# Kernel optimization log

Hardware: AMD Instinct MI355X
Metric: run time of the kernel (lower is better)

Reference implementation:

```python
import jax, jax.numpy as jnp
import numpy as np

B, O, GRID = 2048, 48, 112
SIGMA = 5.0


def setup_inputs() -> dict:
    key = jax.random.key(0)
    k1, k2, k3, k4, k5 = jax.random.split(key, 5)
    s = float(GRID - 1)
    xL = jax.random.uniform(k1, (B,), dtype=jnp.float32) * s
    yL = jax.random.uniform(k2, (B,), dtype=jnp.float32) * s
    obj_list = jax.random.uniform(k3, (B, O, 2), dtype=jnp.float32) * s
    obj_num = jax.random.randint(k4, (B,), 0, O + 1, dtype=jnp.int32)
    road_mask = jax.random.randint(k5, (B, GRID, GRID), 0, 2, dtype=jnp.int32)
    return {"xL": xL, "yL": yL, "obj_list": obj_list, "obj_num": obj_num,
            "road_mask": road_mask, "H": GRID, "W": GRID}


def reference(xL, yL, obj_list, obj_num, road_mask, H, W):
    # Faithful vectorization of batch_gaussian_tensor_obj.
    # exp(-(dx^2+dy^2)/(2s^2)) is separable: exp(-dx^2/..) * exp(-dy^2/..),
    # so per-object splats reduce to a batched matmul over the object axis.
    inv = 1.0 / (2.0 * SIGMA * SIGMA)
    x = jnp.arange(H, dtype=jnp.float32)  # row coordinate grid
    y = jnp.arange(W, dtype=jnp.float32)  # col coordinate grid

    # positive goal gaussian, rank-1 outer product per batch element
    gx = jnp.exp(-((x[None, :] - xL[:, None]) ** 2) * inv)  # [B,H]
    gy = jnp.exp(-((y[None, :] - yL[:, None]) ** 2) * inv)  # [B,W]
    goal = gx[:, :, None] * gy[:, None, :]                   # [B,H,W]

    # negative object gaussians; note original swaps xy: xo=xy[1], yo=xy[0]
    xo = obj_list[:, :, 1]  # [B,O] row coords
    yo = obj_list[:, :, 0]  # [B,O] col coords
    ex = jnp.exp(-((x[None, None, :] - xo[:, :, None]) ** 2) * inv)  # [B,O,H]
    ey = jnp.exp(-((y[None, None, :] - yo[:, :, None]) ** 2) * inv)  # [B,O,W]
    valid = (jnp.arange(O)[None, :] < obj_num[:, None]).astype(jnp.float32)  # [B,O]
    obj = jnp.einsum('boh,bow->bhw', ex * valid[:, :, None], ey)     # [B,H,W]

    channel = 0.5 + 0.5 * goal - 0.5 * obj
    channel = jnp.where(road_mask == 0, 0.0, channel)
    return channel
```

## Files before the change

### kernel.cpp

```cpp
#include <hip/hip_runtime.h>

#define GRID_N 112
#define O_MAX 48
#define HW_N (GRID_N * GRID_N)
#define NT 128
#define ROWS_MAX (O_MAX + 1)

typedef _Float16 half4_t __attribute__((ext_vector_type(4)));
typedef _Float16 half8_t __attribute__((ext_vector_type(8)));

__global__ __launch_bounds__(NT) void goalmap_kernel(
    const float* __restrict__ xL, const float* __restrict__ yL,
    const float* __restrict__ obj_list, const int* __restrict__ obj_num,
    const int* __restrict__ road_mask, float* __restrict__ out)
{
    constexpr float INV = 1.0f / (2.0f * 5.0f * 5.0f);

    __shared__ _Float16 sex[ROWS_MAX * GRID_N];
    __shared__ _Float16 sey[ROWS_MAX * GRID_N];

    const int b   = blockIdx.x;
    const int tid = threadIdx.x;
    const int n   = obj_num[b];
    const int rows = n + 1;
    const float xl = xL[b];
    const float yl = yL[b];

    for (int i = tid; i < rows * GRID_N; i += NT) {
        int o = i / GRID_N;
        int p = i - o * GRID_N;
        float cx, cy, sgn;
        if (o < n) {
            cx  = obj_list[(b * O_MAX + o) * 2 + 1];
            cy  = obj_list[(b * O_MAX + o) * 2 + 0];
            sgn = -0.5f;
        } else {
            cx  = xl;
            cy  = yl;
            sgn = 0.5f;
        }
        float dx = (float)p - cx;
        float dy = (float)p - cy;
        sex[i] = (_Float16)(sgn * __expf(-dx * dx * INV));
        sey[i] = (_Float16)(__expf(-dy * dy * INV));
    }
    __syncthreads();

    const int* rm = road_mask + (size_t)b * HW_N;
    float*     op = out       + (size_t)b * HW_N;

    const int NTILES = (GRID_N / 4) * (GRID_N / 8);
    for (int t = tid; t < NTILES; t += NT) {
        int hp = t / 14;
        int wq = t - hp * 14;
        int h = hp * 4;
        int w = wq * 8;

        float acc[4][8];
        #pragma unroll
        for (int r = 0; r < 4; ++r)
            #pragma unroll
            for (int c = 0; c < 8; ++c) acc[r][c] = 0.f;

        #pragma unroll 2
        for (int o = 0; o < rows; ++o) {
            half4_t ex4 = *(const half4_t*)&sex[o * GRID_N + h];
            half8_t ey8 = *(const half8_t*)&sey[o * GRID_N + w];
            float ef[4], gf[8];
            #pragma unroll
            for (int r = 0; r < 4; ++r) ef[r] = (float)ex4[r];
            #pragma unroll
            for (int c = 0; c < 8; ++c) gf[c] = (float)ey8[c];
            #pragma unroll
            for (int r = 0; r < 4; ++r)
                #pragma unroll
                for (int c = 0; c < 8; ++c)
                    acc[r][c] = fmaf(ef[r], gf[c], acc[r][c]);
        }

        #pragma unroll
        for (int r = 0; r < 4; ++r) {
            int base = (h + r) * GRID_N + w;
            int4 m0 = *(const int4*)&rm[base];
            int4 m1 = *(const int4*)&rm[base + 4];
            float4 v0, v1;
            v0.x = 0.5f + acc[r][0];
            v0.y = 0.5f + acc[r][1];
            v0.z = 0.5f + acc[r][2];
            v0.w = 0.5f + acc[r][3];
            v1.x = 0.5f + acc[r][4];
            v1.y = 0.5f + acc[r][5];
            v1.z = 0.5f + acc[r][6];
            v1.w = 0.5f + acc[r][7];
            v0.x = (m0.x == 0) ? 0.f : v0.x;
            v0.y = (m0.y == 0) ? 0.f : v0.y;
            v0.z = (m0.z == 0) ? 0.f : v0.z;
            v0.w = (m0.w == 0) ? 0.f : v0.w;
            v1.x = (m1.x == 0) ? 0.f : v1.x;
            v1.y = (m1.y == 0) ? 0.f : v1.y;
            v1.z = (m1.z == 0) ? 0.f : v1.z;
            v1.w = (m1.w == 0) ? 0.f : v1.w;
            *(float4*)&op[base]     = v0;
            *(float4*)&op[base + 4] = v1;
        }
    }
}

extern "C" void kernel_launch(void* const* d_in, const int* in_sizes, int n_in,
                              void* d_out, int out_size, void* d_ws, size_t ws_size,
                              hipStream_t stream) {
    const float* xL        = (const float*)d_in[0];
    const float* yL        = (const float*)d_in[1];
    const float* obj_list  = (const float*)d_in[2];
    const int*   obj_num   = (const int*)d_in[3];
    const int*   road_mask = (const int*)d_in[4];
    float*       out       = (float*)d_out;
    const int B = in_sizes[0];

    goalmap_kernel<<<B, NT, 0, stream>>>(xL, yL, obj_list, obj_num, road_mask, out);
}
```

Measured before the change: 222.0 us.

## Compute object splat sum with MFMA 16x16x32 f16 over transposed LDS tiles

Replaces the scalar FMA outer-product accumulation with MFMA matrix instructions. Exponential tables are stored transposed as [position][object] and zero-padded to 64 objects, so each 16x16 output tile takes two MFMA ops. The block size is doubled and work is assigned one tile per wavefront. Every batch element now pays for 64 object slots even when it has few objects, and the stores become scalar per lane, one row segment of 16 floats per quad, which may reduce store coalescing compared with the previous float4 writes.

```diff
diff --git a/kernel.cpp b/kernel.cpp
--- a/kernel.cpp
+++ b/kernel.cpp
@@ -3,11 +3,13 @@
 #define GRID_N 112
 #define O_MAX 48
 #define HW_N (GRID_N * GRID_N)
-#define NT 128
-#define ROWS_MAX (O_MAX + 1)
+#define NT 256
+#define KPAD 64
+#define LSTR 72
 
-typedef _Float16 half4_t __attribute__((ext_vector_type(4)));
-typedef _Float16 half8_t __attribute__((ext_vector_type(8)));
+typedef _Float16 half8  __attribute__((ext_vector_type(8)));
+typedef _Float16 half2v __attribute__((ext_vector_type(2)));
+typedef float    f32x4  __attribute__((ext_vector_type(4)));
 
 __global__ __launch_bounds__(NT) void goalmap_kernel(
     const float* __restrict__ xL, const float* __restrict__ yL,
@@ -16,92 +18,72 @@
 {
     constexpr float INV = 1.0f / (2.0f * 5.0f * 5.0f);
 
-    __shared__ _Float16 sex[ROWS_MAX * GRID_N];
-    __shared__ _Float16 sey[ROWS_MAX * GRID_N];
+    __shared__ _Float16 exT[GRID_N * LSTR];
+    __shared__ _Float16 eyT[GRID_N * LSTR];
 
     const int b   = blockIdx.x;
     const int tid = threadIdx.x;
     const int n   = obj_num[b];
-    const int rows = n + 1;
     const float xl = xL[b];
     const float yl = yL[b];
+    const float* ob = obj_list + (size_t)b * O_MAX * 2;
 
-    for (int i = tid; i < rows * GRID_N; i += NT) {
-        int o = i / GRID_N;
-        int p = i - o * GRID_N;
-        float cx, cy, sgn;
-        if (o < n) {
-            cx  = obj_list[(b * O_MAX + o) * 2 + 1];
-            cy  = obj_list[(b * O_MAX + o) * 2 + 0];
-            sgn = -0.5f;
-        } else {
-            cx  = xl;
-            cy  = yl;
-            sgn = 0.5f;
+    for (int i = tid; i < GRID_N * (KPAD / 2); i += NT) {
+        int pos = i >> 5;
+        int o0  = (i & 31) * 2;
+        half2v vx, vy;
+        #pragma unroll
+        for (int j = 0; j < 2; ++j) {
+            int o = o0 + j;
+            float valx = 0.f, valy = 0.f;
+            if (o <= n) {
+                float cx, cy, s;
+                if (o < n) { cx = ob[o * 2 + 1]; cy = ob[o * 2 + 0]; s = -0.5f; }
+                else       { cx = xl;            cy = yl;            s =  0.5f; }
+                float dx = (float)pos - cx;
+                float dy = (float)pos - cy;
+                valx = s * __expf(-dx * dx * INV);
+                valy =     __expf(-dy * dy * INV);
+            }
+            vx[j] = (_Float16)valx;
+            vy[j] = (_Float16)valy;
         }
-        float dx = (float)p - cx;
-        float dy = (float)p - cy;
-        sex[i] = (_Float16)(sgn * __expf(-dx * dx * INV));
-        sey[i] = (_Float16)(__expf(-dy * dy * INV));
+        *(half2v*)&exT[pos * LSTR + o0] = vx;
+        *(half2v*)&eyT[pos * LSTR + o0] = vy;
     }
     __syncthreads();
 
     const int* rm = road_mask + (size_t)b * HW_N;
     float*     op = out       + (size_t)b * HW_N;
 
-    const int NTILES = (GRID_N / 4) * (GRID_N / 8);
-    for (int t = tid; t < NTILES; t += NT) {
-        int hp = t / 14;
-        int wq = t - hp * 14;
-        int h = hp * 4;
-        int w = wq * 8;
+    const int lane = tid & 63;
+    const int wid  = tid >> 6;
+    const int m    = lane & 15;
+    const int quad = lane >> 4;
 
-        float acc[4][8];
-        #pragma unroll
-        for (int r = 0; r < 4; ++r)
-            #pragma unroll
-            for (int c = 0; c < 8; ++c) acc[r][c] = 0.f;
+    for (int t = wid; t < 49; t += 4) {
+        int th = t / 7;
+        int tw = t - th * 7;
 
-        #pragma unroll 2
-        for (int o = 0; o < rows; ++o) {
-            half4_t ex4 = *(const half4_t*)&sex[o * GRID_N + h];
-            half8_t ey8 = *(const half8_t*)&sey[o * GRID_N + w];
-            float ef[4], gf[8];
-            #pragma unroll
-            for (int r = 0; r < 4; ++r) ef[r] = (float)ex4[r];
-            #pragma unroll
-            for (int c = 0; c < 8; ++c) gf[c] = (float)ey8[c];
-            #pragma unroll
-            for (int r = 0; r < 4; ++r)
-                #pragma unroll
-                for (int c = 0; c < 8; ++c)
-                    acc[r][c] = fmaf(ef[r], gf[c], acc[r][c]);
-        }
+        const _Float16* arow = &exT[(th * 16 + m) * LSTR + quad * 8];
+        const _Float16* brow = &eyT[(tw * 16 + m) * LSTR + quad * 8];
+        half8 a0 = *(const half8*)arow;
+        half8 b0 = *(const half8*)brow;
+        half8 a1 = *(const half8*)(arow + 32);
+        half8 b1 = *(const half8*)(brow + 32);
 
+        f32x4 acc = {0.f, 0.f, 0.f, 0.f};
+        acc = __builtin_amdgcn_mfma_f32_16x16x32_f16(a0, b0, acc, 0, 0, 0);
+        acc = __builtin_amdgcn_mfma_f32_16x16x32_f16(a1, b1, acc, 0, 0, 0);
+
+        int h0 = th * 16 + quad * 4;
+        int w0 = tw * 16 + m;
         #pragma unroll
         for (int r = 0; r < 4; ++r) {
-            int base = (h + r) * GRID_N + w;
-            int4 m0 = *(const int4*)&rm[base];
-            int4 m1 = *(const int4*)&rm[base + 4];
-            float4 v0, v1;
-            v0.x = 0.5f + acc[r][0];
-            v0.y = 0.5f + acc[r][1];
-            v0.z = 0.5f + acc[r][2];
-            v0.w = 0.5f + acc[r][3];
-            v1.x = 0.5f + acc[r][4];
-            v1.y = 0.5f + acc[r][5];
-            v1.z = 0.5f + acc[r][6];
-            v1.w = 0.5f + acc[r][7];
-            v0.x = (m0.x == 0) ? 0.f : v0.x;
-            v0.y = (m0.y == 0) ? 0.f : v0.y;
-            v0.z = (m0.z == 0) ? 0.f : v0.z;
-            v0.w = (m0.w == 0) ? 0.f : v0.w;
-            v1.x = (m1.x == 0) ? 0.f : v1.x;
-            v1.y = (m1.y == 0) ? 0.f : v1.y;
-            v1.z = (m1.z == 0) ? 0.f : v1.z;
-            v1.w = (m1.w == 0) ? 0.f : v1.w;
-            *(float4*)&op[base]     = v0;
-            *(float4*)&op[base + 4] = v1;
+            int idx = (h0 + r) * GRID_N + w0;
+            int mv = rm[idx];
+            float v = 0.5f + acc[r];
+            op[idx] = (mv == 0) ? 0.f : v;
         }
     }
 }
```

Result: no change. 219.6 us (-1.1%).
